# Kernel optimization log

Hardware: AMD Instinct MI355X
Metric: run time of the kernel (lower is better)

## Reference

```python
import jax, jax.numpy as jnp
import numpy as np

N = 8192   # number of points
K = 16     # knn_graph k (loop=True -> self included)
C = 256    # conv hidden width
H = 128    # classifier hidden width


def _lin_init(key, fan_in, fan_out):
    s = 1.0 / np.sqrt(fan_in)
    kw, kb = jax.random.split(key)
    W = jax.random.uniform(kw, (fan_in, fan_out), minval=-s, maxval=s, dtype=jnp.float32)
    b = jax.random.uniform(kb, (fan_out,), minval=-s, maxval=s, dtype=jnp.float32)
    return W, b


def setup_inputs() -> dict:
    key = jax.random.key(0)
    ks = jax.random.split(key, 10)
    pos = jax.random.normal(ks[0], (N, 3), dtype=jnp.float32)
    # conv1 local_nn: Linear(3+3,256), ReLU, Linear(256,256)
    c1_W1, c1_b1 = _lin_init(ks[1], 3 + 3, C)
    c1_W2, c1_b2 = _lin_init(ks[2], C, C)
    # conv2/conv3 local_nn: Linear(256+3,256), ReLU, Linear(256,256)
    c2_W1, c2_b1 = _lin_init(ks[3], C + 3, C)
    c2_W2, c2_b2 = _lin_init(ks[4], C, C)
    c3_W1, c3_b1 = _lin_init(ks[5], C + 3, C)
    c3_W2, c3_b2 = _lin_init(ks[6], C, C)
    # classifier: Linear(256,128), ReLU, Linear(128,128), ReLU, Linear(128,1)
    h_W1, h_b1 = _lin_init(ks[7], C, H)
    h_W2, h_b2 = _lin_init(ks[8], H, H)
    h_W3, h_b3 = _lin_init(ks[9], H, 1)
    return dict(pos=pos,
                c1_W1=c1_W1, c1_b1=c1_b1, c1_W2=c1_W2, c1_b2=c1_b2,
                c2_W1=c2_W1, c2_b1=c2_b1, c2_W2=c2_W2, c2_b2=c2_b2,
                c3_W1=c3_W1, c3_b1=c3_b1, c3_W2=c3_W2, c3_b2=c3_b2,
                h_W1=h_W1, h_b1=h_b1, h_W2=h_W2, h_b2=h_b2, h_W3=h_W3, h_b3=h_b3)


def _knn_idx(pos):
    # squared pairwise distances via the gram trick; [N,N]
    sq = jnp.sum(pos * pos, axis=-1)
    d2 = sq[:, None] + sq[None, :] - 2.0 * (pos @ pos.T)
    # k smallest distances (self distance ~0 -> self loop, matching loop=True)
    _, idx = jax.lax.top_k(-d2, K)  # [N,K] neighbor (source) indices per target
    return idx


def _pointnet_conv(h, rel, idx, W1, b1, W2, b2):
    # message = local_nn(concat(x_j, pos_j - pos_i)); aggregate = max over neighbors
    e = jnp.concatenate([h[idx], rel], axis=-1)          # [N,K,Cin+3]
    m = jax.nn.relu(e @ W1 + b1) @ W2 + b2               # [N,K,C]
    return jnp.max(m, axis=1)                            # [N,C]


def reference(pos,
              c1_W1, c1_b1, c1_W2, c1_b2,
              c2_W1, c2_b1, c2_W2, c2_b2,
              c3_W1, c3_b1, c3_W2, c3_b2,
              h_W1, h_b1, h_W2, h_b2, h_W3, h_b3):
    idx = _knn_idx(pos)
    rel = pos[idx] - pos[:, None, :]                     # [N,K,3] relative coords
    h = pos                                              # train_with_norm=False
    h = jax.nn.relu(_pointnet_conv(h, rel, idx, c1_W1, c1_b1, c1_W2, c1_b2))
    h = jax.nn.relu(_pointnet_conv(h, rel, idx, c2_W1, c2_b1, c2_W2, c2_b2))
    h = jax.nn.relu(_pointnet_conv(h, rel, idx, c3_W1, c3_b1, c3_W2, c3_b2))
    h = jax.nn.relu(h @ h_W1 + h_b1)
    h = jax.nn.relu(h @ h_W2 + h_b2)
    return jax.nn.sigmoid(h @ h_W3 + h_b3)               # [N,1]
```

## Files before the change

### kernel.cpp

```cpp
#include <hip/hip_runtime.h>
#include <hip/hip_bf16.h>
#include <math.h>

#define NPTS 8192
#define CDIM 256
#define HDIM 128
#define NCH  32
#define CH   (NPTS / NCH)
#define CAP  48

typedef __attribute__((ext_vector_type(8))) short bf16x8;
typedef __attribute__((ext_vector_type(4))) float f32x4;
typedef unsigned long long u64;

static __device__ __forceinline__ short f2bf(float f) {
  __hip_bfloat16 h = __float2bfloat16(f);
  return *reinterpret_cast<short*>(&h);
}

static __device__ __forceinline__ unsigned umed3(unsigned a, unsigned b,
                                                 unsigned c) {
  unsigned d;
  asm("v_med3_u32 %0, %1, %2, %3" : "=v"(d) : "v"(a), "v"(b), "v"(c));
  return d;
}

static __device__ __forceinline__ unsigned d2key(float4 p, float4 c) {
  float dot = fmaf(p.x, c.x, fmaf(p.y, c.y, p.z * c.z));
  float d2 = fmaf(-2.0f, dot, p.w + c.w);
  return __float_as_uint(fmaxf(d2, 0.0f));
}

#define U32INIT unsigned b0=~0u,b1=~0u,b2=~0u,b3=~0u,b4=~0u,b5=~0u,b6=~0u, \
                         b7=~0u,b8=~0u,b9=~0u,b10=~0u,b11=~0u,b12=~0u, \
                         b13=~0u,b14=~0u,b15=~0u;
#define U32CHAIN(key) { \
  b15 = umed3(b14, key, b15); b14 = umed3(b13, key, b14); \
  b13 = umed3(b12, key, b13); b12 = umed3(b11, key, b12); \
  b11 = umed3(b10, key, b11); b10 = umed3(b9,  key, b10); \
  b9  = umed3(b8,  key, b9);  b8  = umed3(b7,  key, b8);  \
  b7  = umed3(b6,  key, b7);  b6  = umed3(b5,  key, b6);  \
  b5  = umed3(b4,  key, b5);  b4  = umed3(b3,  key, b4);  \
  b3  = umed3(b2,  key, b3);  b2  = umed3(b1,  key, b2);  \
  b1  = umed3(b0,  key, b1);  b0  = min(b0, key); }

#define KSTEP(s) { bool sw_ = key < k##s; u64 t_ = k##s; \
                   k##s = sw_ ? key : t_; key = sw_ ? t_ : key; }
#define KCHAIN KSTEP(0) KSTEP(1) KSTEP(2) KSTEP(3) KSTEP(4) KSTEP(5) \
               KSTEP(6) KSTEP(7) KSTEP(8) KSTEP(9) KSTEP(10) KSTEP(11) \
               KSTEP(12) KSTEP(13) KSTEP(14) KSTEP(15)
#define KINIT u64 k0=~0ULL,k1=~0ULL,k2=~0ULL,k3=~0ULL,k4=~0ULL,k5=~0ULL, \
                  k6=~0ULL,k7=~0ULL,k8=~0ULL,k9=~0ULL,k10=~0ULL,k11=~0ULL, \
                  k12=~0ULL,k13=~0ULL,k14=~0ULL,k15=~0ULL;

__global__ __launch_bounds__(256) void prep_all(
    const float* __restrict__ c1W2, const float* __restrict__ c2W2,
    const float* __restrict__ c3W2, const float* __restrict__ c2W1,
    const float* __restrict__ c3W1, const float* __restrict__ hW1,
    const float* __restrict__ hW2,
    short* __restrict__ w2f1, short* __restrict__ w2f2,
    short* __restrict__ w2f3, short* __restrict__ wc2a,
    short* __restrict__ wc3a, short* __restrict__ whW1,
    short* __restrict__ whW2,
    const float* __restrict__ pos, float4* __restrict__ pos4,
    const float* __restrict__ c1W1, const float* __restrict__ c1b1,
    float* __restrict__ TU) {
  int b = blockIdx.x, tid = threadIdx.x;
  if (b < 1280) {
    const float* W; short* wf; int rb;
    if (b < 256)       { W = c1W2; wf = w2f1; rb = b; }
    else if (b < 512)  { W = c2W2; wf = w2f2; rb = b - 256; }
    else if (b < 768)  { W = c3W2; wf = w2f3; rb = b - 512; }
    else if (b < 1024) { W = c2W1; wf = wc2a; rb = b - 768; }
    else               { W = c3W1; wf = wc3a; rb = b - 1024; }
    int t = rb * 256 + tid;
    int q = t & 7, l = (t >> 3) & 63, F = t >> 9;
    int ks = F & 7, c16 = F >> 3;
    int k = ks * 32 + ((l >> 4) << 3) + q;
    int c = c16 * 16 + (l & 15);
    wf[t] = f2bf(W[k * 256 + c]);
  } else if (b < 1408) {
    int t = (b - 1280) * 256 + tid;
    int q = t & 7, l = (t >> 3) & 63, F = t >> 9;
    int ks = F & 7, c16 = F >> 3;
    int k = ks * 32 + ((l >> 4) << 3) + q;
    int c = c16 * 16 + (l & 15);
    whW1[t] = f2bf(hW1[k * 128 + c]);
  } else if (b < 1472) {
    int t = (b - 1408) * 256 + tid;
    int q = t & 7, l = (t >> 3) & 63, F = t >> 9;
    int ks = F & 3, c16 = F >> 2;
    int k = ks * 32 + ((l >> 4) << 3) + q;
    int c = c16 * 16 + (l & 15);
    whW2[t] = f2bf(hW2[k * 128 + c]);
  } else if (b < 1504) {
    int i = (b - 1472) * 256 + tid;
    float x = pos[3 * i], y = pos[3 * i + 1], z = pos[3 * i + 2];
    pos4[i] = make_float4(x, y, z, x * x + y * y + z * z);
  } else {
    int c = tid;
    float w0 = c1W1[c]       + c1W1[768 + c];
    float w1 = c1W1[256 + c] + c1W1[1024 + c];
    float w2 = c1W1[512 + c] + c1W1[1280 + c];
    float bv = c1b1[c];
    int i0 = (b - 1504) * 16;
#pragma unroll
    for (int r = 0; r < 16; ++r) {
      int i = i0 + r;
      float x = pos[3 * i], y = pos[3 * i + 1], z = pos[3 * i + 2];
      TU[(size_t)i * 256 + c] = fmaf(x, w0, fmaf(y, w1, fmaf(z, w2, bv)));
    }
  }
}

__global__ __launch_bounds__(256) void knn_d2p1(const float4* __restrict__ pos4,
                                                unsigned* __restrict__ v) {
  __shared__ float4 cand[CH];
  int ch = blockIdx.x & (NCH - 1);
  int i  = (blockIdx.x >> 5) * 256 + threadIdx.x;
  cand[threadIdx.x] = pos4[ch * CH + threadIdx.x];
  __syncthreads();

  float4 p = pos4[i];
  U32INIT
  for (int jj = 0; jj < CH; jj += 4) {
    float4 c0 = cand[jj], c1 = cand[jj + 1], c2 = cand[jj + 2],
           c3 = cand[jj + 3];
    unsigned x0 = d2key(p, c0), x1 = d2key(p, c1);
    unsigned x2 = d2key(p, c2), x3 = d2key(p, c3);
    U32CHAIN(x0) U32CHAIN(x1) U32CHAIN(x2) U32CHAIN(x3)
  }
  uint4* dst = reinterpret_cast<uint4*>(v + ((size_t)ch * NPTS + i) * 16);
  dst[0] = make_uint4(b0, b1, b2, b3);
  dst[1] = make_uint4(b4, b5, b6, b7);
  dst[2] = make_uint4(b8, b9, b10, b11);
  dst[3] = make_uint4(b12, b13, b14, b15);
}

__global__ __launch_bounds__(256) void knn_merge(const unsigned* __restrict__ v,
                                                 unsigned* __restrict__ T,
                                                 unsigned* __restrict__ cnt) {
  int wv = threadIdx.x >> 6, lane = threadIdx.x & 63;
  int i = blockIdx.x * 4 + wv;
  int ch = lane >> 1, half = lane & 1;
  const uint4* src = reinterpret_cast<const uint4*>(
      v + ((size_t)ch * NPTS + i) * 16 + half * 8);
  uint4 a = src[0], b = src[1];
  unsigned r1 = a.y, r2 = a.z, r3 = a.w;
  unsigned r4 = b.x, r5 = b.y, r6 = b.z, r7 = b.w;
  unsigned h = a.x;
  int idx = 0;
  unsigned wmin = 0;
#pragma unroll
  for (int round = 0; round < 16; ++round) {
    unsigned m = h;
    m = min(m, (unsigned)__shfl_xor((int)m, 1));
    m = min(m, (unsigned)__shfl_xor((int)m, 2));
    m = min(m, (unsigned)__shfl_xor((int)m, 4));
    m = min(m, (unsigned)__shfl_xor((int)m, 8));
    m = min(m, (unsigned)__shfl_xor((int)m, 16));
    m = min(m, (unsigned)__shfl_xor((int)m, 32));
    wmin = m;
    u64 ball = __ballot(h == m);
    int src_lane = __ffsll(ball) - 1;
    if (lane == src_lane) {
      ++idx;
      h = idx == 1 ? r1 : idx == 2 ? r2 : idx == 3 ? r3 : idx == 4 ? r4 :
          idx == 5 ? r5 : idx == 6 ? r6 : idx == 7 ? r7 : 0xFFFFFFFFu;
    }
  }
  if (lane == 0) { T[i] = wmin; cnt[i] = 0; }
}

__global__ __launch_bounds__(256) void knn_d2p2(const float4* __restrict__ pos4,
                                                const unsigned* __restrict__ T,
                                                unsigned* __restrict__ cnt,
                                                u64* __restrict__ cbuf) {
  __shared__ float4 cand[CH];
  int ch = blockIdx.x & (NCH - 1);
  int i  = (blockIdx.x >> 5) * 256 + threadIdx.x;
  cand[threadIdx.x] = pos4[ch * CH + threadIdx.x];
  __syncthreads();

  float4 p = pos4[i];
  unsigned Ti = T[i];
  int jb = ch * CH;
  for (int jj = 0; jj < CH; jj += 8) {
    unsigned k[8];
#pragma unroll
    for (int u = 0; u < 8; ++u) k[u] = d2key(p, cand[jj + u]);
    unsigned m = min(min(min(k[0], k[1]), min(k[2], k[3])),
                     min(min(k[4], k[5]), min(k[6], k[7])));
    if (m <= Ti) {
#pragma unroll
      for (int u = 0; u < 8; ++u) {
        if (k[u] <= Ti) {
          unsigned slot = atomicAdd(&cnt[i], 1u);
          if (slot < CAP)
            cbuf[(size_t)i * CAP + slot] =
                ((u64)k[u] << 32) | (unsigned)(jb + jj + u);
        }
      }
    }
  }
}

__global__ __launch_bounds__(256) void knn_select(const unsigned* __restrict__ cnt,
                                                  const u64* __restrict__ cbuf,
                                                  int* __restrict__ idx_out) {
  int i = blockIdx.x * 256 + threadIdx.x;
  int c = (int)min(cnt[i], (unsigned)CAP);
  KINIT
#pragma unroll 1
  for (int q = 0; q < c; ++q) {
    u64 key = cbuf[(size_t)i * CAP + q];
    if (key < k15) { KCHAIN }
  }
  int* o = idx_out + i * 16;
  o[0]=(int)(unsigned)k0;   o[1]=(int)(unsigned)k1;   o[2]=(int)(unsigned)k2;
  o[3]=(int)(unsigned)k3;   o[4]=(int)(unsigned)k4;   o[5]=(int)(unsigned)k5;
  o[6]=(int)(unsigned)k6;   o[7]=(int)(unsigned)k7;   o[8]=(int)(unsigned)k8;
  o[9]=(int)(unsigned)k9;   o[10]=(int)(unsigned)k10; o[11]=(int)(unsigned)k11;
  o[12]=(int)(unsigned)k12; o[13]=(int)(unsigned)k13; o[14]=(int)(unsigned)k14;
  o[15]=(int)(unsigned)k15;
}

template <int NCOLS, int KDIM, int ACT, int ADDP>
__global__ __launch_bounds__(256) void gemm_mfma(
    const float* __restrict__ A,
    const short* __restrict__ wf,
    const float* __restrict__ bias,
    const float* __restrict__ pos,
    const float* __restrict__ W1p,
    float* __restrict__ out) {
  constexpr int KS = KDIM / 32;
  constexpr int NF = NCOLS / 64;
  __shared__ __align__(16) short As[32 * KDIM];

  int tid = threadIdx.x;
  int row0 = blockIdx.x * 32;

  {
    int row = tid & 31, wq = tid >> 5;
    const float* Ar = A + (size_t)(row0 + row) * KDIM;
#pragma unroll
    for (int q = 0; q < KDIM / 64; ++q) {
      int c0 = wq * 8 + q * 64;
      float4 a = *reinterpret_cast<const float4*>(Ar + c0);
      float4 b = *reinterpret_cast<const float4*>(Ar + c0 + 4);
      bf16x8 o;
      o[0] = f2bf(a.x); o[1] = f2bf(a.y); o[2] = f2bf(a.z); o[3] = f2bf(a.w);
      o[4] = f2bf(b.x); o[5] = f2bf(b.y); o[6] = f2bf(b.z); o[7] = f2bf(b.w);
      int byte = row * (KDIM * 2) + c0 * 2;
      byte ^= (row & 7) << 4;
      *reinterpret_cast<bf16x8*>(reinterpret_cast<char*>(As) + byte) = o;
    }
  }
  __syncthreads();

  int l = tid & 63, w = tid >> 6;
  int lhi = l >> 4, llo = l & 15;
  f32x4 zero = {0.f, 0.f, 0.f, 0.f};
  f32x4 acc[2][NF];
#pragma unroll
  for (int m = 0; m < 2; ++m)
#pragma unroll
    for (int n = 0; n < NF; ++n) acc[m][n] = zero;

  const bf16x8* WfV = reinterpret_cast<const bf16x8*>(wf);
#pragma unroll
  for (int ks = 0; ks < KS; ++ks) {
    bf16x8 af[2], bfr[NF];
#pragma unroll
    for (int m = 0; m < 2; ++m) {
      int r = m * 16 + llo;
      int byte = r * (KDIM * 2) + ks * 64 + lhi * 16;
      byte ^= (r & 7) << 4;
      af[m] = *reinterpret_cast<const bf16x8*>(
          reinterpret_cast<const char*>(As) + byte);
    }
#pragma unroll
    for (int n = 0; n < NF; ++n)
      bfr[n] = WfV[((w * NF + n) * KS + ks) * 64 + l];
#pragma unroll
    for (int m = 0; m < 2; ++m)
#pragma unroll
      for (int n = 0; n < NF; ++n)
        acc[m][n] = __builtin_amdgcn_mfma_f32_16x16x32_bf16(af[m], bfr[n],
                                                            acc[m][n], 0, 0, 0);
  }

  int cc[NF];
  float bv[NF], u0[NF], u1[NF], u2[NF];
#pragma unroll
  for (int n = 0; n < NF; ++n) {
    cc[n] = (w * NF + n) * 16 + llo;
    bv[n] = bias[cc[n]];
    if constexpr (ADDP) {
      u0[n] = W1p[cc[n]];
      u1[n] = W1p[NCOLS + cc[n]];
      u2[n] = W1p[2 * NCOLS + cc[n]];
    } else { u0[n] = u1[n] = u2[n] = 0.f; }
  }
#pragma unroll
  for (int m = 0; m < 2; ++m)
#pragma unroll
    for (int j = 0; j < 4; ++j) {
      int r = row0 + m * 16 + lhi * 4 + j;
      float px = 0.f, py = 0.f, pz = 0.f;
      if constexpr (ADDP) { px = pos[3*r]; py = pos[3*r+1]; pz = pos[3*r+2]; }
#pragma unroll
      for (int n = 0; n < NF; ++n) {
        float v = acc[m][n][j] + bv[n];
        if constexpr (ADDP) v += px * u0[n] + py * u1[n] + pz * u2[n];
        if (ACT == 1) v = fmaxf(v, 0.0f);
        out[(size_t)r * NCOLS + cc[n]] = v;
      }
    }
}

__global__ __launch_bounds__(256) void conv_mfma(
    const float* __restrict__ TU,
    const float* __restrict__ pos,
    const int* __restrict__ idx,
    const float* __restrict__ W1p,
    const short* __restrict__ w2f,
    const float* __restrict__ b2,
    float* __restrict__ hout) {
  __shared__ __align__(16) short m1s[64 * 256];
  __shared__ float Ub[4][256];
  __shared__ int js[64];

  int tid = threadIdx.x;
  int t0 = blockIdx.x * 4;
  if (tid < 64) js[tid] = idx[(t0 + (tid >> 4)) * 16 + (tid & 15)];
#pragma unroll
  for (int q = 0; q < 4; ++q) {
    int e = tid + 256 * q;
    int tg = e >> 8, c = e & 255;
    float x = pos[3 * (t0 + tg)], y = pos[3 * (t0 + tg) + 1],
          z = pos[3 * (t0 + tg) + 2];
    Ub[tg][c] = x * W1p[c] + y * W1p[256 + c] + z * W1p[512 + c];
  }
  __syncthreads();

  {
    int row = tid & 63;
    int wq = tid >> 6;
    int jrow = js[row];
    const float* TUj = TU + (size_t)jrow * 256;
    const float* Ui = &Ub[row >> 4][0];
#pragma unroll
    for (int q = 0; q < 8; ++q) {
      int c0 = wq * 8 + q * 32;
      float4 a = *reinterpret_cast<const float4*>(TUj + c0);
      float4 b = *reinterpret_cast<const float4*>(TUj + c0 + 4);
      float4 ua = *reinterpret_cast<const float4*>(Ui + c0);
      float4 ub = *reinterpret_cast<const float4*>(Ui + c0 + 4);
      bf16x8 o;
      o[0] = f2bf(fmaxf(a.x - ua.x, 0.f));
      o[1] = f2bf(fmaxf(a.y - ua.y, 0.f));
      o[2] = f2bf(fmaxf(a.z - ua.z, 0.f));
      o[3] = f2bf(fmaxf(a.w - ua.w, 0.f));
      o[4] = f2bf(fmaxf(b.x - ub.x, 0.f));
      o[5] = f2bf(fmaxf(b.y - ub.y, 0.f));
      o[6] = f2bf(fmaxf(b.z - ub.z, 0.f));
      o[7] = f2bf(fmaxf(b.w - ub.w, 0.f));
      int byte = row * 512 + c0 * 2;
      byte ^= (row & 7) << 4;
      *reinterpret_cast<bf16x8*>(reinterpret_cast<char*>(m1s) + byte) = o;
    }
  }
  __syncthreads();

  int l = tid & 63, w = tid >> 6;
  int lhi = l >> 4, llo = l & 15;
  f32x4 zero = {0.f, 0.f, 0.f, 0.f};
  f32x4 acc[4][4];
#pragma unroll
  for (int m = 0; m < 4; ++m)
#pragma unroll
    for (int n = 0; n < 4; ++n) acc[m][n] = zero;

  const bf16x8* Wf = reinterpret_cast<const bf16x8*>(w2f);
#pragma unroll
  for (int ks = 0; ks < 8; ++ks) {
    int k0 = ks * 32;
    bf16x8 af[4], bfr[4];
#pragma unroll
    for (int m = 0; m < 4; ++m) {
      int r = m * 16 + llo;
      int byte = r * 512 + k0 * 2 + lhi * 16;
      byte ^= (r & 7) << 4;
      af[m] = *reinterpret_cast<const bf16x8*>(
          reinterpret_cast<const char*>(m1s) + byte);
    }
#pragma unroll
    for (int n = 0; n < 4; ++n)
      bfr[n] = Wf[((w * 4 + n) * 8 + ks) * 64 + l];
#pragma unroll
    for (int m = 0; m < 4; ++m)
#pragma unroll
      for (int n = 0; n < 4; ++n)
        acc[m][n] = __builtin_amdgcn_mfma_f32_16x16x32_bf16(af[m], bfr[n],
                                                            acc[m][n], 0, 0, 0);
  }

#pragma unroll
  for (int m = 0; m < 4; ++m)
#pragma unroll
    for (int n = 0; n < 4; ++n) {
      float v = fmaxf(fmaxf(acc[m][n][0], acc[m][n][1]),
                      fmaxf(acc[m][n][2], acc[m][n][3]));
      v = fmaxf(v, __shfl_xor(v, 16));
      v = fmaxf(v, __shfl_xor(v, 32));
      if (lhi == 0) {
        int c = w * 64 + n * 16 + llo;
        hout[(size_t)(t0 + m) * CDIM + c] = fmaxf(v + b2[c], 0.0f);
      }
    }
}

__global__ __launch_bounds__(64) void final_k(const float* __restrict__ h2,
                                              const float* __restrict__ w3,
                                              const float* __restrict__ b3,
                                              float* __restrict__ out) {
  int r = blockIdx.x, l = threadIdx.x;
  float s = h2[(size_t)r * HDIM + l] * w3[l] +
            h2[(size_t)r * HDIM + 64 + l] * w3[64 + l];
#pragma unroll
  for (int o = 32; o > 0; o >>= 1) s += __shfl_down(s, o);
  if (l == 0) out[r] = 1.0f / (1.0f + expf(-(s + b3[0])));
}

extern "C" void kernel_launch(void* const* d_in, const int* in_sizes, int n_in,
                              void* d_out, int out_size, void* d_ws,
                              size_t ws_size, hipStream_t stream) {
  const float* pos   = (const float*)d_in[0];
  const float* c1_W1 = (const float*)d_in[1];
  const float* c1_b1 = (const float*)d_in[2];
  const float* c1_W2 = (const float*)d_in[3];
  const float* c1_b2 = (const float*)d_in[4];
  const float* c2_W1 = (const float*)d_in[5];
  const float* c2_b1 = (const float*)d_in[6];
  const float* c2_W2 = (const float*)d_in[7];
  const float* c2_b2 = (const float*)d_in[8];
  const float* c3_W1 = (const float*)d_in[9];
  const float* c3_b1 = (const float*)d_in[10];
  const float* c3_W2 = (const float*)d_in[11];
  const float* c3_b2 = (const float*)d_in[12];
  const float* h_W1  = (const float*)d_in[13];
  const float* h_b1  = (const float*)d_in[14];
  const float* h_W2  = (const float*)d_in[15];
  const float* h_b2  = (const float*)d_in[16];
  const float* h_W3  = (const float*)d_in[17];
  const float* h_b3  = (const float*)d_in[18];
  float* out = (float*)d_out;

  char* w = (char*)d_ws;
  const size_t MB = 1 << 20;
  const size_t KB = 1 << 10;
  int*      p_idx  = (int*)w;
  float4*   p_pos4 = (float4*)(w + 512 * KB);
  unsigned* p_T    = (unsigned*)(w + 640 * KB);
  unsigned* p_cnt  = (unsigned*)(w + 672 * KB);
  short*    p_w2f1 = (short*)(w + 704 * KB);
  short*    p_w2f2 = (short*)(w + 832 * KB);
  short*    p_w2f3 = (short*)(w + 960 * KB);
  short*    p_wc2a = (short*)(w + 1088 * KB);
  short*    p_wc3a = (short*)(w + 1216 * KB);
  short*    p_whW1 = (short*)(w + 1344 * KB);
  short*    p_whW2 = (short*)(w + 1408 * KB);
  u64*      p_cbuf = (u64*)(w + 1536 * KB);
  float*    p_TU   = (float*)(w + 5 * MB);
  unsigned* p_v    = (unsigned*)(w + 13 * MB);
  float*    p_hA   = (float*)(w + 13 * MB);
  float*    p_hB   = (float*)(w + 21 * MB);
  float*    p_c1   = (float*)(w + 5 * MB);
  float*    p_c2   = (float*)(w + 9 * MB);

  prep_all<<<2016, 256, 0, stream>>>(
      c1_W2, c2_W2, c3_W2, c2_W1, c3_W1, h_W1, h_W2,
      p_w2f1, p_w2f2, p_w2f3, p_wc2a, p_wc3a, p_whW1, p_whW2,
      pos, p_pos4, c1_W1, c1_b1, p_TU);

  knn_d2p1<<<(NPTS / 256) * NCH, 256, 0, stream>>>(p_pos4, p_v);
  knn_merge<<<NPTS / 4, 256, 0, stream>>>(p_v, p_T, p_cnt);
  knn_d2p2<<<(NPTS / 256) * NCH, 256, 0, stream>>>(p_pos4, p_T, p_cnt, p_cbuf);
  knn_select<<<NPTS / 256, 256, 0, stream>>>(p_cnt, p_cbuf, p_idx);

  conv_mfma<<<NPTS / 4, 256, 0, stream>>>(p_TU, pos, p_idx, c1_W1 + 3 * 256,
                                          p_w2f1, c1_b2, p_hA);
  gemm_mfma<256, 256, 0, 1><<<NPTS / 32, 256, 0, stream>>>(
      p_hA, p_wc2a, c2_b1, pos, c2_W1 + 256 * 256, p_TU);
  conv_mfma<<<NPTS / 4, 256, 0, stream>>>(p_TU, pos, p_idx, c2_W1 + 256 * 256,
                                          p_w2f2, c2_b2, p_hB);
  gemm_mfma<256, 256, 0, 1><<<NPTS / 32, 256, 0, stream>>>(
      p_hB, p_wc3a, c3_b1, pos, c3_W1 + 256 * 256, p_TU);
  conv_mfma<<<NPTS / 4, 256, 0, stream>>>(p_TU, pos, p_idx, c3_W1 + 256 * 256,
                                          p_w2f3, c3_b2, p_hA);
  gemm_mfma<128, 256, 1, 0><<<NPTS / 32, 256, 0, stream>>>(
      p_hA, p_whW1, h_b1, nullptr, nullptr, p_c1);
  gemm_mfma<128, 128, 1, 0><<<NPTS / 32, 256, 0, stream>>>(
      p_c1, p_whW2, h_b2, nullptr, nullptr, p_c2);
  final_k<<<NPTS, 64, 0, stream>>>(p_c2, h_W3, h_b3, out);

  (void)in_sizes; (void)n_in; (void)out_size; (void)ws_size;
}
```

Measured before the change: 289.7 us.

## Sort points by x-bucket and split kNN candidate scan across two thread halves

Adds a histogram/scan/scatter pass that reorders points by x-coordinate bucket, so the whole pipeline runs in sorted order, with index remapping in knn_select and a scatter back to original order in final_k. The kNN pass kernels now handle 128 targets per block, with each half of the block scanning half of the candidate chunk and merging through shared memory. The sorted order is meant to improve gather locality in the conv kernels and tighten the pass-1 thresholds, and the halved scan doubles parallelism. In exchange it adds four small launches and global atomics.

```diff
diff --git a/kernel.cpp b/kernel.cpp
--- a/kernel.cpp
+++ b/kernel.cpp
@@ -8,6 +8,7 @@
 #define NCH  32
 #define CH   (NPTS / NCH)
 #define CAP  48
+#define NBKT 256
 
 typedef __attribute__((ext_vector_type(8))) short bf16x8;
 typedef __attribute__((ext_vector_type(4))) float f32x4;
@@ -29,6 +30,11 @@
   float dot = fmaf(p.x, c.x, fmaf(p.y, c.y, p.z * c.z));
   float d2 = fmaf(-2.0f, dot, p.w + c.w);
   return __float_as_uint(fmaxf(d2, 0.0f));
+}
+
+static __device__ __forceinline__ int xbucket(float x) {
+  int b = (int)floorf((x + 4.0f) * 32.0f);
+  return min(max(b, 0), NBKT - 1);
 }
 
 #define U32INIT unsigned b0=~0u,b1=~0u,b2=~0u,b3=~0u,b4=~0u,b5=~0u,b6=~0u, \
@@ -62,9 +68,7 @@
     short* __restrict__ w2f3, short* __restrict__ wc2a,
     short* __restrict__ wc3a, short* __restrict__ whW1,
     short* __restrict__ whW2,
-    const float* __restrict__ pos, float4* __restrict__ pos4,
-    const float* __restrict__ c1W1, const float* __restrict__ c1b1,
-    float* __restrict__ TU) {
+    unsigned* __restrict__ hist, unsigned* __restrict__ cursor) {
   int b = blockIdx.x, tid = threadIdx.x;
   if (b < 1280) {
     const float* W; short* wf; int rb;
@@ -93,48 +97,88 @@
     int k = ks * 32 + ((l >> 4) << 3) + q;
     int c = c16 * 16 + (l & 15);
     whW2[t] = f2bf(hW2[k * 128 + c]);
-  } else if (b < 1504) {
-    int i = (b - 1472) * 256 + tid;
-    float x = pos[3 * i], y = pos[3 * i + 1], z = pos[3 * i + 2];
-    pos4[i] = make_float4(x, y, z, x * x + y * y + z * z);
   } else {
-    int c = tid;
-    float w0 = c1W1[c]       + c1W1[768 + c];
-    float w1 = c1W1[256 + c] + c1W1[1024 + c];
-    float w2 = c1W1[512 + c] + c1W1[1280 + c];
-    float bv = c1b1[c];
-    int i0 = (b - 1504) * 16;
-#pragma unroll
-    for (int r = 0; r < 16; ++r) {
-      int i = i0 + r;
-      float x = pos[3 * i], y = pos[3 * i + 1], z = pos[3 * i + 2];
-      TU[(size_t)i * 256 + c] = fmaf(x, w0, fmaf(y, w1, fmaf(z, w2, bv)));
-    }
-  }
+    hist[tid] = 0u;
+    cursor[tid] = 0u;
+  }
+}
+
+__global__ __launch_bounds__(256) void hist_k(const float* __restrict__ pos,
+                                              unsigned* __restrict__ hist) {
+  int i = blockIdx.x * 256 + threadIdx.x;
+  atomicAdd(&hist[xbucket(pos[3 * i])], 1u);
+}
+
+__global__ __launch_bounds__(256) void scan_k(const unsigned* __restrict__ hist,
+                                              unsigned* __restrict__ base) {
+  __shared__ unsigned s[NBKT];
+  int t = threadIdx.x;
+  unsigned h = hist[t];
+  s[t] = h;
+  __syncthreads();
+  for (int off = 1; off < NBKT; off <<= 1) {
+    unsigned v = (t >= off) ? s[t - off] : 0u;
+    __syncthreads();
+    s[t] += v;
+    __syncthreads();
+  }
+  base[t] = s[t] - h;
+}
+
+__global__ __launch_bounds__(256) void scatter_k(
+    const float* __restrict__ pos, const unsigned* __restrict__ base,
+    unsigned* __restrict__ cursor, int* __restrict__ sidx,
+    int* __restrict__ inv, float4* __restrict__ pos4) {
+  int i = blockIdx.x * 256 + threadIdx.x;
+  float x = pos[3 * i], y = pos[3 * i + 1], z = pos[3 * i + 2];
+  int b = xbucket(x);
+  unsigned slot = base[b] + atomicAdd(&cursor[b], 1u);
+  sidx[slot] = i;
+  inv[i] = (int)slot;
+  pos4[slot] = make_float4(x, y, z, x * x + y * y + z * z);
 }
 
 __global__ __launch_bounds__(256) void knn_d2p1(const float4* __restrict__ pos4,
                                                 unsigned* __restrict__ v) {
   __shared__ float4 cand[CH];
+  __shared__ unsigned mbuf[128][16];
   int ch = blockIdx.x & (NCH - 1);
-  int i  = (blockIdx.x >> 5) * 256 + threadIdx.x;
-  cand[threadIdx.x] = pos4[ch * CH + threadIdx.x];
+  int tgp = blockIdx.x >> 5;
+  int tid = threadIdx.x;
+  int i = tgp * 128 + (tid & 127);
+  int half = tid >> 7;
+  cand[tid] = pos4[ch * CH + tid];
   __syncthreads();
 
   float4 p = pos4[i];
   U32INIT
-  for (int jj = 0; jj < CH; jj += 4) {
-    float4 c0 = cand[jj], c1 = cand[jj + 1], c2 = cand[jj + 2],
-           c3 = cand[jj + 3];
+  int j0 = half * 128;
+  for (int jj = 0; jj < 128; jj += 4) {
+    float4 c0 = cand[j0 + jj],     c1 = cand[j0 + jj + 1];
+    float4 c2 = cand[j0 + jj + 2], c3 = cand[j0 + jj + 3];
     unsigned x0 = d2key(p, c0), x1 = d2key(p, c1);
     unsigned x2 = d2key(p, c2), x3 = d2key(p, c3);
     U32CHAIN(x0) U32CHAIN(x1) U32CHAIN(x2) U32CHAIN(x3)
   }
-  uint4* dst = reinterpret_cast<uint4*>(v + ((size_t)ch * NPTS + i) * 16);
-  dst[0] = make_uint4(b0, b1, b2, b3);
-  dst[1] = make_uint4(b4, b5, b6, b7);
-  dst[2] = make_uint4(b8, b9, b10, b11);
-  dst[3] = make_uint4(b12, b13, b14, b15);
+  if (half) {
+    unsigned* m = mbuf[tid - 128];
+    m[0]=b0; m[1]=b1; m[2]=b2;  m[3]=b3;  m[4]=b4;  m[5]=b5;  m[6]=b6;  m[7]=b7;
+    m[8]=b8; m[9]=b9; m[10]=b10;m[11]=b11;m[12]=b12;m[13]=b13;m[14]=b14;m[15]=b15;
+  }
+  __syncthreads();
+  if (!half) {
+#pragma unroll 1
+    for (int s = 0; s < 16; ++s) {
+      unsigned key = mbuf[tid][s];
+      if (key >= b15) break;
+      U32CHAIN(key)
+    }
+    uint4* dst = reinterpret_cast<uint4*>(v + ((size_t)ch * NPTS + i) * 16);
+    dst[0] = make_uint4(b0, b1, b2, b3);
+    dst[1] = make_uint4(b4, b5, b6, b7);
+    dst[2] = make_uint4(b8, b9, b10, b11);
+    dst[3] = make_uint4(b12, b13, b14, b15);
+  }
 }
 
 __global__ __launch_bounds__(256) void knn_merge(const unsigned* __restrict__ v,
@@ -173,22 +217,28 @@
 }
 
 __global__ __launch_bounds__(256) void knn_d2p2(const float4* __restrict__ pos4,
+                                                const int* __restrict__ sidx,
                                                 const unsigned* __restrict__ T,
                                                 unsigned* __restrict__ cnt,
                                                 u64* __restrict__ cbuf) {
   __shared__ float4 cand[CH];
+  __shared__ int sj[CH];
   int ch = blockIdx.x & (NCH - 1);
-  int i  = (blockIdx.x >> 5) * 256 + threadIdx.x;
-  cand[threadIdx.x] = pos4[ch * CH + threadIdx.x];
+  int tgp = blockIdx.x >> 5;
+  int tid = threadIdx.x;
+  int i = tgp * 128 + (tid & 127);
+  int half = tid >> 7;
+  cand[tid] = pos4[ch * CH + tid];
+  sj[tid] = sidx[ch * CH + tid];
   __syncthreads();
 
   float4 p = pos4[i];
   unsigned Ti = T[i];
-  int jb = ch * CH;
-  for (int jj = 0; jj < CH; jj += 8) {
+  int j0 = half * 128;
+  for (int jj = 0; jj < 128; jj += 8) {
     unsigned k[8];
 #pragma unroll
-    for (int u = 0; u < 8; ++u) k[u] = d2key(p, cand[jj + u]);
+    for (int u = 0; u < 8; ++u) k[u] = d2key(p, cand[j0 + jj + u]);
     unsigned m = min(min(min(k[0], k[1]), min(k[2], k[3])),
                      min(min(k[4], k[5]), min(k[6], k[7])));
     if (m <= Ti) {
@@ -198,7 +248,7 @@
           unsigned slot = atomicAdd(&cnt[i], 1u);
           if (slot < CAP)
             cbuf[(size_t)i * CAP + slot] =
-                ((u64)k[u] << 32) | (unsigned)(jb + jj + u);
+                ((u64)k[u] << 32) | (unsigned)sj[j0 + jj + u];
         }
       }
     }
@@ -207,6 +257,7 @@
 
 __global__ __launch_bounds__(256) void knn_select(const unsigned* __restrict__ cnt,
                                                   const u64* __restrict__ cbuf,
+                                                  const int* __restrict__ inv,
                                                   int* __restrict__ idx_out) {
   int i = blockIdx.x * 256 + threadIdx.x;
   int c = (int)min(cnt[i], (unsigned)CAP);
@@ -217,12 +268,29 @@
     if (key < k15) { KCHAIN }
   }
   int* o = idx_out + i * 16;
-  o[0]=(int)(unsigned)k0;   o[1]=(int)(unsigned)k1;   o[2]=(int)(unsigned)k2;
-  o[3]=(int)(unsigned)k3;   o[4]=(int)(unsigned)k4;   o[5]=(int)(unsigned)k5;
-  o[6]=(int)(unsigned)k6;   o[7]=(int)(unsigned)k7;   o[8]=(int)(unsigned)k8;
-  o[9]=(int)(unsigned)k9;   o[10]=(int)(unsigned)k10; o[11]=(int)(unsigned)k11;
-  o[12]=(int)(unsigned)k12; o[13]=(int)(unsigned)k13; o[14]=(int)(unsigned)k14;
-  o[15]=(int)(unsigned)k15;
+  o[0]=inv[(unsigned)k0];   o[1]=inv[(unsigned)k1];   o[2]=inv[(unsigned)k2];
+  o[3]=inv[(unsigned)k3];   o[4]=inv[(unsigned)k4];   o[5]=inv[(unsigned)k5];
+  o[6]=inv[(unsigned)k6];   o[7]=inv[(unsigned)k7];   o[8]=inv[(unsigned)k8];
+  o[9]=inv[(unsigned)k9];   o[10]=inv[(unsigned)k10]; o[11]=inv[(unsigned)k11];
+  o[12]=inv[(unsigned)k12]; o[13]=inv[(unsigned)k13]; o[14]=inv[(unsigned)k14];
+  o[15]=inv[(unsigned)k15];
+}
+
+__global__ __launch_bounds__(256) void tu1_prep(const float4* __restrict__ pos4,
+                                                const float* __restrict__ W1,
+                                                const float* __restrict__ b1,
+                                                float* __restrict__ TU) {
+  int c = threadIdx.x;
+  float w0 = W1[c]       + W1[768 + c];
+  float w1 = W1[256 + c] + W1[1024 + c];
+  float w2 = W1[512 + c] + W1[1280 + c];
+  float bv = b1[c];
+#pragma unroll
+  for (int r = 0; r < 4; ++r) {
+    int i = blockIdx.x * 4 + r;
+    float4 P = pos4[i];
+    TU[(size_t)i * 256 + c] = fmaf(P.x, w0, fmaf(P.y, w1, fmaf(P.z, w2, bv)));
+  }
 }
 
 template <int NCOLS, int KDIM, int ACT, int ADDP>
@@ -230,7 +298,7 @@
     const float* __restrict__ A,
     const short* __restrict__ wf,
     const float* __restrict__ bias,
-    const float* __restrict__ pos,
+    const float4* __restrict__ pos4,
     const float* __restrict__ W1p,
     float* __restrict__ out) {
   constexpr int KS = KDIM / 32;
@@ -308,7 +376,10 @@
     for (int j = 0; j < 4; ++j) {
       int r = row0 + m * 16 + lhi * 4 + j;
       float px = 0.f, py = 0.f, pz = 0.f;
-      if constexpr (ADDP) { px = pos[3*r]; py = pos[3*r+1]; pz = pos[3*r+2]; }
+      if constexpr (ADDP) {
+        float4 P = pos4[r];
+        px = P.x; py = P.y; pz = P.z;
+      }
 #pragma unroll
       for (int n = 0; n < NF; ++n) {
         float v = acc[m][n][j] + bv[n];
@@ -321,7 +392,7 @@
 
 __global__ __launch_bounds__(256) void conv_mfma(
     const float* __restrict__ TU,
-    const float* __restrict__ pos,
+    const float4* __restrict__ pos4,
     const int* __restrict__ idx,
     const float* __restrict__ W1p,
     const short* __restrict__ w2f,
@@ -338,9 +409,8 @@
   for (int q = 0; q < 4; ++q) {
     int e = tid + 256 * q;
     int tg = e >> 8, c = e & 255;
-    float x = pos[3 * (t0 + tg)], y = pos[3 * (t0 + tg) + 1],
-          z = pos[3 * (t0 + tg) + 2];
-    Ub[tg][c] = x * W1p[c] + y * W1p[256 + c] + z * W1p[512 + c];
+    float4 P = pos4[t0 + tg];
+    Ub[tg][c] = P.x * W1p[c] + P.y * W1p[256 + c] + P.z * W1p[512 + c];
   }
   __syncthreads();
 
@@ -424,13 +494,14 @@
 __global__ __launch_bounds__(64) void final_k(const float* __restrict__ h2,
                                               const float* __restrict__ w3,
                                               const float* __restrict__ b3,
+                                              const int* __restrict__ sidx,
                                               float* __restrict__ out) {
   int r = blockIdx.x, l = threadIdx.x;
   float s = h2[(size_t)r * HDIM + l] * w3[l] +
             h2[(size_t)r * HDIM + 64 + l] * w3[64 + l];
 #pragma unroll
   for (int o = 32; o > 0; o >>= 1) s += __shfl_down(s, o);
-  if (l == 0) out[r] = 1.0f / (1.0f + expf(-(s + b3[0])));
+  if (l == 0) out[sidx[r]] = 1.0f / (1.0f + expf(-(s + b3[0])));
 }
 
 extern "C" void kernel_launch(void* const* d_in, const int* in_sizes, int n_in,
@@ -471,6 +542,11 @@
   short*    p_wc3a = (short*)(w + 1216 * KB);
   short*    p_whW1 = (short*)(w + 1344 * KB);
   short*    p_whW2 = (short*)(w + 1408 * KB);
+  unsigned* p_hist = (unsigned*)(w + 1440 * KB);
+  unsigned* p_base = (unsigned*)(w + 1441 * KB);
+  unsigned* p_cur  = (unsigned*)(w + 1442 * KB);
+  int*      p_sidx = (int*)(w + 1444 * KB);
+  int*      p_inv  = (int*)(w + 1476 * KB);
   u64*      p_cbuf = (u64*)(w + 1536 * KB);
   float*    p_TU   = (float*)(w + 5 * MB);
   unsigned* p_v    = (unsigned*)(w + 13 * MB);
@@ -479,31 +555,38 @@
   float*    p_c1   = (float*)(w + 5 * MB);
   float*    p_c2   = (float*)(w + 9 * MB);
 
-  prep_all<<<2016, 256, 0, stream>>>(
+  prep_all<<<1473, 256, 0, stream>>>(
       c1_W2, c2_W2, c3_W2, c2_W1, c3_W1, h_W1, h_W2,
-      p_w2f1, p_w2f2, p_w2f3, p_wc2a, p_wc3a, p_whW1, p_whW2,
-      pos, p_pos4, c1_W1, c1_b1, p_TU);
-
-  knn_d2p1<<<(NPTS / 256) * NCH, 256, 0, stream>>>(p_pos4, p_v);
+      p_w2f1, p_w2f2, p_w2f3, p_wc2a, p_wc3a, p_whW1, p_whW2, p_hist, p_cur);
+
+  hist_k<<<NPTS / 256, 256, 0, stream>>>(pos, p_hist);
+  scan_k<<<1, 256, 0, stream>>>(p_hist, p_base);
+  scatter_k<<<NPTS / 256, 256, 0, stream>>>(pos, p_base, p_cur,
+                                            p_sidx, p_inv, p_pos4);
+
+  tu1_prep<<<NPTS / 4, 256, 0, stream>>>(p_pos4, c1_W1, c1_b1, p_TU);
+
+  knn_d2p1<<<(NPTS / 128) * NCH, 256, 0, stream>>>(p_pos4, p_v);
   knn_merge<<<NPTS / 4, 256, 0, stream>>>(p_v, p_T, p_cnt);
-  knn_d2p2<<<(NPTS / 256) * NCH, 256, 0, stream>>>(p_pos4, p_T, p_cnt, p_cbuf);
-  knn_select<<<NPTS / 256, 256, 0, stream>>>(p_cnt, p_cbuf, p_idx);
-
-  conv_mfma<<<NPTS / 4, 256, 0, stream>>>(p_TU, pos, p_idx, c1_W1 + 3 * 256,
+  knn_d2p2<<<(NPTS / 128) * NCH, 256, 0, stream>>>(p_pos4, p_sidx, p_T,
+                                                   p_cnt, p_cbuf);
+  knn_select<<<NPTS / 256, 256, 0, stream>>>(p_cnt, p_cbuf, p_inv, p_idx);
+
+  conv_mfma<<<NPTS / 4, 256, 0, stream>>>(p_TU, p_pos4, p_idx, c1_W1 + 3 * 256,
                                           p_w2f1, c1_b2, p_hA);
   gemm_mfma<256, 256, 0, 1><<<NPTS / 32, 256, 0, stream>>>(
-      p_hA, p_wc2a, c2_b1, pos, c2_W1 + 256 * 256, p_TU);
-  conv_mfma<<<NPTS / 4, 256, 0, stream>>>(p_TU, pos, p_idx, c2_W1 + 256 * 256,
-                                          p_w2f2, c2_b2, p_hB);
+      p_hA, p_wc2a, c2_b1, p_pos4, c2_W1 + 256 * 256, p_TU);
+  conv_mfma<<<NPTS / 4, 256, 0, stream>>>(p_TU, p_pos4, p_idx,
+                                          c2_W1 + 256 * 256, p_w2f2, c2_b2, p_hB);
   gemm_mfma<256, 256, 0, 1><<<NPTS / 32, 256, 0, stream>>>(
-      p_hB, p_wc3a, c3_b1, pos, c3_W1 + 256 * 256, p_TU);
-  conv_mfma<<<NPTS / 4, 256, 0, stream>>>(p_TU, pos, p_idx, c3_W1 + 256 * 256,
-                                          p_w2f3, c3_b2, p_hA);
+      p_hB, p_wc3a, c3_b1, p_pos4, c3_W1 + 256 * 256, p_TU);
+  conv_mfma<<<NPTS / 4, 256, 0, stream>>>(p_TU, p_pos4, p_idx,
+                                          c3_W1 + 256 * 256, p_w2f3, c3_b2, p_hA);
   gemm_mfma<128, 256, 1, 0><<<NPTS / 32, 256, 0, stream>>>(
       p_hA, p_whW1, h_b1, nullptr, nullptr, p_c1);
   gemm_mfma<128, 128, 1, 0><<<NPTS / 32, 256, 0, stream>>>(
       p_c1, p_whW2, h_b2, nullptr, nullptr, p_c2);
-  final_k<<<NPTS, 64, 0, stream>>>(p_c2, h_W3, h_b3, out);
+  final_k<<<NPTS, 64, 0, stream>>>(p_c2, h_W3, h_b3, p_sidx, out);
 
   (void)in_sizes; (void)n_in; (void)out_size; (void)ws_size;
 }
```

Result: slower. 308.9 us (+6.6%).
